# Kernel optimization log

Measured on AMD Instinct MI355X. Metric: run time of the kernel, lower is better.

The kernel has to match this reference:

```python
import jax, jax.numpy as jnp
import numpy as np

B, C, T = 8, 512, 1024
EXP = 2
E = EXP * C          # 1024, gate/value width
H, HD = 8, 64        # heads, qk head dim
QK = H * HD          # 512
AVG_LEN = 512
EPS = 1e-5


def setup_inputs() -> dict:
    key = jax.random.key(0)
    ks = jax.random.split(key, 10)
    s = 0.02
    return {
        "x": jax.random.normal(ks[0], (B, C, T), jnp.float32),
        "W_in": jax.random.normal(ks[1], (2 * E, C), jnp.float32) * s,
        "b_in": jnp.zeros((2 * E,), jnp.float32),
        "W_attn": jax.random.normal(ks[2], (QK, C), jnp.float32) * s,
        "b_attn": jnp.zeros((QK,), jnp.float32),
        "w_q": 1.0 + jax.random.normal(ks[3], (QK,), jnp.float32) * 0.1,
        "b_q": jax.random.normal(ks[4], (QK,), jnp.float32) * 0.1,
        "w_k": 1.0 + jax.random.normal(ks[5], (QK,), jnp.float32) * 0.1,
        "b_k": jax.random.normal(ks[6], (QK,), jnp.float32) * 0.1,
        "W_out": jax.random.normal(ks[7], (C, E), jnp.float32) * s,
        "b_out": jnp.zeros((C,), jnp.float32),
        "gamma": jnp.ones((C,), jnp.float32),
    }


def reference(x, W_in, b_in, W_attn, b_attn, w_q, b_q, w_k, b_k, W_out, b_out, gamma):
    residual = x
    # mlp_in (1x1 conv) + SiLU, then chunk into gate u and value v, each (B,E,T)
    uv = jax.nn.silu(jnp.einsum('oc,bct->bot', W_in, x) + b_in[:, None])
    u, v = uv[:, :E], uv[:, E:]
    # mlp_attn (1x1 conv); no activation (activation_attn unused in forward)
    z = jnp.einsum('oc,bct->bot', W_attn, x) + b_attn[:, None]  # (B,QK,T)
    # depthwise 1x1 conv on cat(z,z) = two independent per-channel affines
    q = z * w_q[:, None] + b_q[:, None]
    k = z * w_k[:, None] + b_k[:, None]
    # split heads: q,k -> (B,H,T,HD); v -> (B,H,T,E//H)
    q = q.reshape(B, H, HD, T).transpose(0, 1, 3, 2)
    k = k.reshape(B, H, HD, T).transpose(0, 1, 3, 2)
    vh = v.reshape(B, H, E // H, T).transpose(0, 1, 3, 2)
    # entropy-invariant scale: (log n / log avg_len) / sqrt(d)
    scale = (np.log(T) / np.log(AVG_LEN)) / np.sqrt(HD)
    scores = jnp.einsum('bhqd,bhkd->bhqk', q, k) * jnp.float32(scale)
    attn = jax.nn.softmax(scores, axis=-1)
    o = jnp.einsum('bhqk,bhke->bhqe', attn, vh)        # (B,H,T,E//H)
    o = o.transpose(0, 1, 3, 2).reshape(B, E, T)       # back to (B,E,T)
    # gate, project out, residual + RMSNorm over channel dim
    out = jnp.einsum('ce,bet->bct', W_out, u * o) + b_out[:, None]
    y = residual + out
    rms = jax.lax.rsqrt(jnp.mean(y * y, axis=1, keepdims=True) + EPS)
    return y * rms * gamma[:, None]
```

## Files before the change

kernel.cpp:

```cpp
#include <hip/hip_runtime.h>

typedef __attribute__((ext_vector_type(8))) short short8;
typedef __attribute__((ext_vector_type(4))) float f32x4;
typedef __attribute__((ext_vector_type(16))) float f32x16;

__device__ __forceinline__ unsigned short f2b(float f) {
  union { float f; unsigned u; } x; x.f = f;
  unsigned r = (x.u + 0x7fffu + ((x.u >> 16) & 1u)) >> 16;
  return (unsigned short)r;
}
__device__ __forceinline__ float b2f(unsigned short b) {
  union { unsigned u; float f; } x; x.u = ((unsigned)b) << 16;
  return x.f;
}
__device__ __forceinline__ unsigned cvtpk(float lo, float hi) {
  unsigned r;
  asm("v_cvt_pk_bf16_f32 %0, %1, %2" : "=v"(r) : "v"(lo), "v"(hi));
  return r;
}
__device__ __forceinline__ void plswap(unsigned& a, unsigned& b) {
  asm volatile("v_permlane32_swap_b32 %0, %1" : "+v"(a), "+v"(b));
}

#define GLDS16(gp, lp)                                                                  \
  __builtin_amdgcn_global_load_lds((const __attribute__((address_space(1))) void*)(gp), \
                                   (__attribute__((address_space(3))) void*)(lp), 16, 0, 0)

__global__ __launch_bounds__(256) void prep_kernel(const float* __restrict__ x,
                                                   const float* __restrict__ W_in,
                                                   const float* __restrict__ W_attn,
                                                   const float* __restrict__ W_out,
                                                   unsigned short* __restrict__ Wcat,
                                                   unsigned short* __restrict__ WoutB,
                                                   unsigned short* __restrict__ xT) {
  if (blockIdx.x < 4096) {
    __shared__ float tile[32][33];
    const int bid = blockIdx.x;
    const int b = bid & 7;
    const int rem = bid >> 3;
    const int c0 = (rem >> 5) << 5;
    const int t0 = (rem & 31) << 5;
    const int tj = threadIdx.x & 31, ti = threadIdx.x >> 5;
#pragma unroll
    for (int r = 0; r < 32; r += 8)
      tile[ti + r][tj] = x[(((size_t)b << 9) + c0 + ti + r) * 1024 + t0 + tj];
    __syncthreads();
#pragma unroll
    for (int r = 0; r < 32; r += 8)
      xT[(((size_t)b << 10) + t0 + ti + r) * 512 + c0 + tj] = f2b(tile[tj][ti + r]);
  } else {
    const int n1 = 2048 * 512, n2 = 512 * 512, n3 = 512 * 1024;
    for (int i = (blockIdx.x - 4096) * 256 + threadIdx.x; i < n1 + n2 + n3; i += 896 * 256) {
      if (i < n1) Wcat[i] = f2b(W_in[i]);
      else if (i < n1 + n2) Wcat[i] = f2b(W_attn[i - n1]);
      else WoutB[i - n1 - n2] = f2b(W_out[i - n1 - n2]);
    }
  }
}

__device__ __forceinline__ void gemm_stage(const unsigned short* Ag, const unsigned short* Bg,
                                           int lda, int ldb, int k0, unsigned short* lsA,
                                           unsigned short* lsB, int buf, int sr, int sk,
                                           int ldst) {
  const int bb = buf * 8192;
  GLDS16(Ag + (size_t)sr * lda + k0 + sk, (char*)lsA + bb + ldst);
  GLDS16(Ag + (size_t)(sr + 64) * lda + k0 + sk, (char*)lsA + bb + 4096 + ldst);
  GLDS16(Bg + (size_t)sr * ldb + k0 + sk, (char*)lsB + bb + ldst);
  GLDS16(Bg + (size_t)(sr + 64) * ldb + k0 + sk, (char*)lsB + bb + 4096 + ldst);
}

__device__ __forceinline__ void gemm_bt_core(const unsigned short* __restrict__ Ag,
                                             const unsigned short* __restrict__ Bg, int lda,
                                             int ldb, int K, unsigned short* lsA,
                                             unsigned short* lsB, f32x4 acc[4][4]) {
  const int tid = threadIdx.x;
  const int lane = tid & 63;
  const int w = tid >> 6;
  const int wr = w >> 1, wc = w & 1;
  const int sr = tid >> 2;
  const int sk = (((tid & 3) ^ ((sr >> 1) & 3)) << 3);
  const int ldst = (tid >> 6) << 10;

  const int nt = K >> 5;
  int c0b = 0, c1b = 1, c2b = 2;
  gemm_stage(Ag, Bg, lda, ldb, 0, lsA, lsB, 0, sr, sk, ldst);
  gemm_stage(Ag, Bg, lda, ldb, 32, lsA, lsB, 1, sr, sk, ldst);
  for (int t = 0; t < nt; ++t) {
    if (t + 1 < nt) {
      asm volatile("s_waitcnt vmcnt(4)" ::: "memory");
    } else {
      asm volatile("s_waitcnt vmcnt(0)" ::: "memory");
    }
    __builtin_amdgcn_s_barrier();
    if (t + 2 < nt)
      gemm_stage(Ag, Bg, lda, ldb, (t + 2) << 5, lsA, lsB, c2b, sr, sk, ldst);
    short8 af[4], bfr[4];
    const int bb = c0b * 8192;
    const int ko = (lane >> 4) << 4;
    const int ra = (wr << 6) + (lane & 15);
    const int rb = (wc << 6) + (lane & 15);
#pragma unroll
    for (int mi = 0; mi < 4; ++mi) {
      const int rowA = ra + (mi << 4);
      af[mi] = *(const short8*)((const char*)lsA + bb + (rowA << 6) +
                                (ko ^ (((rowA >> 1) & 3) << 4)));
    }
#pragma unroll
    for (int ni = 0; ni < 4; ++ni) {
      const int rowB = rb + (ni << 4);
      bfr[ni] = *(const short8*)((const char*)lsB + bb + (rowB << 6) +
                                 (ko ^ (((rowB >> 1) & 3) << 4)));
    }
#pragma unroll
    for (int mi = 0; mi < 4; ++mi)
#pragma unroll
      for (int ni = 0; ni < 4; ++ni)
        acc[mi][ni] =
            __builtin_amdgcn_mfma_f32_16x16x32_bf16(af[mi], bfr[ni], acc[mi][ni], 0, 0, 0);
    const int tmp = c0b; c0b = c1b; c1b = c2b; c2b = tmp;
  }
}

__global__ __launch_bounds__(256) void gemm_a_kernel(
    const unsigned short* __restrict__ Wcat, const unsigned short* __restrict__ xT,
    const float* __restrict__ b_in, const float* __restrict__ b_attn,
    const float* __restrict__ w_q, const float* __restrict__ b_q, const float* __restrict__ w_k,
    const float* __restrict__ b_k, unsigned short* __restrict__ u, unsigned short* __restrict__ v,
    unsigned short* __restrict__ qT, unsigned short* __restrict__ kT) {
  __shared__ __align__(16) unsigned short lsA[12288];
  __shared__ __align__(16) unsigned short lsB[12288];
  const int bid = ((blockIdx.x & 7) * 160) + (blockIdx.x >> 3);
  const int b = bid / 160;
  const int rem = bid % 160;
  const int m0 = (rem >> 3) << 7;
  const int n0 = (rem & 7) << 7;
  f32x4 acc[4][4];
  const f32x4 z4 = {0.f, 0.f, 0.f, 0.f};
#pragma unroll
  for (int mi = 0; mi < 4; ++mi)
#pragma unroll
    for (int ni = 0; ni < 4; ++ni) acc[mi][ni] = z4;

  const unsigned short* Ag = Wcat + (size_t)m0 * 512;
  const unsigned short* Bg = xT + ((size_t)b << 19) + ((size_t)n0 << 9);
  gemm_bt_core(Ag, Bg, 512, 512, 512, lsA, lsB, acc);

  const int lane = threadIdx.x & 63;
  const int w = threadIdx.x >> 6;
  const int wr = w >> 1, wc = w & 1;
#pragma unroll
  for (int mi = 0; mi < 4; ++mi) {
    const int row0 = m0 + (wr << 6) + (mi << 4) + ((lane >> 4) << 2);
#pragma unroll
    for (int ni = 0; ni < 4; ++ni) {
      const int col = n0 + (wc << 6) + (ni << 4) + (lane & 15);
      if (row0 < 2048) {
#pragma unroll
        for (int i = 0; i < 4; ++i) {
          const int row = row0 + i;
          const float s = acc[mi][ni][i] + b_in[row];
          const float r = s / (1.f + __expf(-s));
          if (row < 1024)
            u[((((size_t)b << 10) + row) << 10) + col] = f2b(r);
          else
            v[((((size_t)b << 10) + (row - 1024)) << 10) + col] = f2b(r);
        }
      } else {
        const int c0 = row0 - 2048;
        ushort4 qv, kv;
        unsigned short* qp = (unsigned short*)&qv;
        unsigned short* kp = (unsigned short*)&kv;
#pragma unroll
        for (int i = 0; i < 4; ++i) {
          const int c = c0 + i;
          const float z = acc[mi][ni][i] + b_attn[c];
          qp[i] = f2b(z * w_q[c] + b_q[c]);
          kp[i] = f2b(z * w_k[c] + b_k[c]);
        }
        const int h = c0 >> 6, d = c0 & 63;
        const size_t base = ((((size_t)b * 8 + h) << 10) + col) * 64 + d;
        *(ushort4*)(qT + base) = qv;
        *(ushort4*)(kT + base) = kv;
      }
    }
  }
}

__global__ __launch_bounds__(256, 2) void attn_kernel(const unsigned short* __restrict__ qT,
                                                      const unsigned short* __restrict__ kT,
                                                      const unsigned short* __restrict__ v,
                                                      const unsigned short* __restrict__ u,
                                                      unsigned short* __restrict__ uoT) {
  __shared__ __align__(16) unsigned short Kls[3 * 4096];
  __shared__ __align__(16) unsigned short Vls[3 * 8192];
  const float SCALE2 = 0.20037430567f;
  const int bx = blockIdx.x;
  const int xcd = bx & 7, idx = bx >> 3;
  const int bh = (xcd << 3) + (idx & 7);
  const int qb = idx >> 3;
  const int b = bh >> 3, h = bh & 7;
  const int tid = threadIdx.x;
  const int lane = tid & 63;
  const int w = tid >> 6;
  const int l5 = lane >> 5;
  const int l31 = lane & 31;
  const int q0 = qb << 7;

  const unsigned short* qh = qT + ((size_t)bh << 16);
  const unsigned short* kh = kT + ((size_t)bh << 16);
  const unsigned short* vh = v + ((((size_t)b << 10) + (h << 7)) << 10);

  short8 qf[4];
#pragma unroll
  for (int ds = 0; ds < 4; ++ds)
    qf[ds] = *(const short8*)(qh + (size_t)(q0 + (w << 5) + l31) * 64 + (ds << 4) + (l5 << 3));

  f32x16 o[4];
#pragma unroll
  for (int eb = 0; eb < 4; ++eb)
#pragma unroll
    for (int i = 0; i < 16; ++i) o[eb][i] = 0.f;
  float lacc = 0.f;

  const int srow = tid >> 3;
  const int scol = (((tid & 7) ^ (srow & 7)) << 3);

#define ATTN_STAGE(buf, kt)                                                            \
  {                                                                                    \
    const int t2 = (kt) << 6;                                                          \
    char* kbase = (char*)Kls + (buf)*8192;                                             \
    char* vbase = (char*)Vls + (buf)*16384;                                            \
    GLDS16(kh + (size_t)(t2 + srow) * 64 + scol, kbase + (w << 10));                   \
    GLDS16(kh + (size_t)(t2 + 32 + srow) * 64 + scol, kbase + 4096 + (w << 10));       \
    GLDS16(vh + ((size_t)srow << 10) + t2 + scol, vbase + (w << 10));                  \
    GLDS16(vh + ((size_t)(32 + srow) << 10) + t2 + scol, vbase + 4096 + (w << 10));    \
    GLDS16(vh + ((size_t)(64 + srow) << 10) + t2 + scol, vbase + 8192 + (w << 10));    \
    GLDS16(vh + ((size_t)(96 + srow) << 10) + t2 + scol, vbase + 12288 + (w << 10));   \
  }

#define KREAD(kbp, kr, ds)                                                             \
  (*(const short8*)((kbp) + ((kr) << 7) + ((((ds) << 5) + (l5 << 4)) ^ (((kr)&7) << 4))))
#define VREAD(vbp, vrow, ks)                                                           \
  (*(const short8*)((vbp) + ((vrow) << 7) + ((((ks) << 5) + (l5 << 4)) ^ (((vrow)&7) << 4))))

#define PACK(sv, out0, out1)                                                           \
  do {                                                                                 \
    float p_[16];                                                                      \
    _Pragma("unroll") for (int i_ = 0; i_ < 16; ++i_) {                                \
      p_[i_] = exp2f(sv[i_] * SCALE2);                                                 \
      lacc += p_[i_];                                                                  \
    }                                                                                  \
    unsigned W00 = cvtpk(p_[0], p_[1]), W01 = cvtpk(p_[2], p_[3]);                     \
    unsigned W10 = cvtpk(p_[4], p_[5]), W11 = cvtpk(p_[6], p_[7]);                     \
    unsigned W20 = cvtpk(p_[8], p_[9]), W21 = cvtpk(p_[10], p_[11]);                   \
    unsigned W30 = cvtpk(p_[12], p_[13]), W31 = cvtpk(p_[14], p_[15]);                 \
    unsigned a_ = W10, b_ = W00;                                                       \
    plswap(a_, b_);                                                                    \
    (out0).u4[0] = b_; (out0).u4[2] = a_;                                              \
    unsigned c_ = W11, d_ = W01;                                                       \
    plswap(c_, d_);                                                                    \
    (out0).u4[1] = d_; (out0).u4[3] = c_;                                              \
    unsigned e_ = W30, f_ = W20;                                                       \
    plswap(e_, f_);                                                                    \
    (out1).u4[0] = f_; (out1).u4[2] = e_;                                              \
    unsigned g_ = W31, h_ = W21;                                                       \
    plswap(g_, h_);                                                                    \
    (out1).u4[1] = h_; (out1).u4[3] = g_;                                              \
  } while (0)

  union U8 { short8 s8; unsigned u4[4]; };
  U8 pfP[4];

  ATTN_STAGE(0, 0);
  ATTN_STAGE(1, 1);

  asm volatile("s_waitcnt vmcnt(6)" ::: "memory");
  __builtin_amdgcn_s_barrier();
  {
    const char* kb = (const char*)Kls;
    f32x16 s0, s1;
#pragma unroll
    for (int i = 0; i < 16; ++i) { s0[i] = 0.f; s1[i] = 0.f; }
    __builtin_amdgcn_s_setprio(1);
#pragma unroll
    for (int ds = 0; ds < 4; ++ds) {
      short8 kfA = KREAD(kb, l31, ds);
      s0 = __builtin_amdgcn_mfma_f32_32x32x16_bf16(kfA, qf[ds], s0, 0, 0, 0);
      short8 kfB = KREAD(kb, 32 + l31, ds);
      s1 = __builtin_amdgcn_mfma_f32_32x32x16_bf16(kfB, qf[ds], s1, 0, 0, 0);
    }
    __builtin_amdgcn_s_setprio(0);
    PACK(s0, pfP[0], pfP[1]);
    PACK(s1, pfP[2], pfP[3]);
  }
  __builtin_amdgcn_s_barrier();
  ATTN_STAGE(2, 2);

  int ck = 1, cv = 0;
  for (int kt = 1; kt < 16; ++kt) {
    if (kt < 15) {
      asm volatile("s_waitcnt vmcnt(6)" ::: "memory");
    } else {
      asm volatile("s_waitcnt vmcnt(0)" ::: "memory");
    }
    __builtin_amdgcn_s_barrier();

    const char* kb = (const char*)Kls + ck * 8192;
    const char* vb = (const char*)Vls + cv * 16384;

    short8 kfA[4], kfB[4];
#pragma unroll
    for (int ds = 0; ds < 4; ++ds) {
      kfA[ds] = KREAD(kb, l31, ds);
      kfB[ds] = KREAD(kb, 32 + l31, ds);
    }

    f32x16 s0, s1;
#pragma unroll
    for (int i = 0; i < 16; ++i) { s0[i] = 0.f; s1[i] = 0.f; }
    __builtin_amdgcn_s_setprio(1);
#pragma unroll
    for (int ks = 0; ks < 4; ++ks) {
      s0 = __builtin_amdgcn_mfma_f32_32x32x16_bf16(kfA[ks], qf[ks], s0, 0, 0, 0);
      s1 = __builtin_amdgcn_mfma_f32_32x32x16_bf16(kfB[ks], qf[ks], s1, 0, 0, 0);
#pragma unroll
      for (int eb = 0; eb < 4; ++eb) {
        short8 vf = VREAD(vb, (eb << 5) + l31, ks);
        o[eb] = __builtin_amdgcn_mfma_f32_32x32x16_bf16(vf, pfP[ks].s8, o[eb], 0, 0, 0);
      }
    }
    __builtin_amdgcn_s_setprio(0);

    U8 pfN[4];
    PACK(s0, pfN[0], pfN[1]);
    PACK(s1, pfN[2], pfN[3]);
#pragma unroll
    for (int i = 0; i < 4; ++i) pfP[i] = pfN[i];

    if (kt + 2 < 16) {
      __builtin_amdgcn_s_barrier();
      ATTN_STAGE(cv, kt + 2);
    }
    const int third = 3 - ck - cv;
    cv = ck;
    ck = third;
  }

  {
    const char* vb = (const char*)Vls + cv * 16384;
    __builtin_amdgcn_s_setprio(1);
#pragma unroll
    for (int ks = 0; ks < 4; ++ks) {
#pragma unroll
      for (int eb = 0; eb < 4; ++eb) {
        short8 vf = VREAD(vb, (eb << 5) + l31, ks);
        o[eb] = __builtin_amdgcn_mfma_f32_32x32x16_bf16(vf, pfP[ks].s8, o[eb], 0, 0, 0);
      }
    }
    __builtin_amdgcn_s_setprio(0);
  }
#undef ATTN_STAGE
#undef KREAD
#undef VREAD
#undef PACK

  lacc += __shfl_xor(lacc, 32, 64);
  const float rl = 1.f / lacc;
  const int t = q0 + (w << 5) + l31;

#pragma unroll
  for (int eb = 0; eb < 4; ++eb) {
#pragma unroll
    for (int g = 0; g < 4; ++g) {
      const int e4 = (eb << 5) + (g << 3) + (l5 << 2);
      const int eg = (h << 7) + e4;
      ushort4 outv;
      unsigned short* op = (unsigned short*)&outv;
#pragma unroll
      for (int j = 0; j < 4; ++j) {
        const int i = (g << 2) + j;
        const float oo = o[eb][i] * rl;
        const float uu = b2f(u[((((size_t)b << 10) + eg + j) << 10) + t]);
        op[j] = f2b(oo * uu);
      }
      *(ushort4*)(uoT + ((((size_t)b << 10) + t) << 10) + eg) = outv;
    }
  }
}

__global__ __launch_bounds__(256) void gemm_c_kernel(const unsigned short* __restrict__ uoT,
                                                     const unsigned short* __restrict__ WoutB,
                                                     const float* __restrict__ x,
                                                     const float* __restrict__ b_out,
                                                     unsigned short* __restrict__ y) {
  __shared__ __align__(16) unsigned short lsA[12288];
  __shared__ __align__(16) unsigned short lsB[12288];
  const int bid = ((blockIdx.x & 7) * 32) + (blockIdx.x >> 3);
  const int b = bid >> 5;
  const int rem = bid & 31;
  const int m0 = (rem >> 2) << 7;
  const int n0 = (rem & 3) << 7;
  f32x4 acc[4][4];
  const f32x4 z4 = {0.f, 0.f, 0.f, 0.f};
#pragma unroll
  for (int mi = 0; mi < 4; ++mi)
#pragma unroll
    for (int ni = 0; ni < 4; ++ni) acc[mi][ni] = z4;

  const unsigned short* Ag = uoT + ((size_t)b << 20) + ((size_t)m0 << 10);
  const unsigned short* Bg = WoutB + ((size_t)n0 << 10);
  gemm_bt_core(Ag, Bg, 1024, 1024, 1024, lsA, lsB, acc);

  const int lane = threadIdx.x & 63;
  const int w = threadIdx.x >> 6;
  const int wr = w >> 1, wc = w & 1;
#pragma unroll
  for (int mi = 0; mi < 4; ++mi) {
    const int t4 = m0 + (wr << 6) + (mi << 4) + ((lane >> 4) << 2);
#pragma unroll
    for (int ni = 0; ni < 4; ++ni) {
      const int c = n0 + (wc << 6) + (ni << 4) + (lane & 15);
      const size_t base = ((((size_t)b << 9) + c) << 10) + t4;
      const f32x4 xv = *(const f32x4*)(x + base);
      const float bo = b_out[c];
      ushort4 ov;
      unsigned short* op = (unsigned short*)&ov;
#pragma unroll
      for (int i = 0; i < 4; ++i) op[i] = f2b(acc[mi][ni][i] + bo + xv[i]);
      *(ushort4*)(y + base) = ov;
    }
  }
}

__global__ __launch_bounds__(256) void rms_kernel(const unsigned short* __restrict__ y,
                                                  const float* __restrict__ gamma,
                                                  float* __restrict__ out) {
  __shared__ float part[8][32];
  __shared__ float rmsv[32];
  const int bid = blockIdx.x;
  const int b = bid >> 5;
  const int t0 = (bid & 31) << 5;
  const int tid = threadIdx.x;
  const int tt = tid & 31, cg = tid >> 5;
  const int t = t0 + tt;
  float vals[64];
  float ss = 0.f;
#pragma unroll
  for (int ci = 0; ci < 64; ++ci) {
    const int c = (cg << 6) + ci;
    const float vv = b2f(y[((((size_t)b << 9) + c) << 10) + t]);
    vals[ci] = vv;
    ss += vv * vv;
  }
  part[cg][tt] = ss;
  __syncthreads();
  if (tid < 32) {
    float tot = 0.f;
#pragma unroll
    for (int g = 0; g < 8; ++g) tot += part[g][tid];
    rmsv[tid] = rsqrtf(tot / 512.f + 1e-5f);
  }
  __syncthreads();
  const float rm = rmsv[tt];
#pragma unroll
  for (int ci = 0; ci < 64; ++ci) {
    const int c = (cg << 6) + ci;
    out[((((size_t)b << 9) + c) << 10) + t] = vals[ci] * rm * gamma[c];
  }
}

extern "C" void kernel_launch(void* const* d_in, const int* in_sizes, int n_in, void* d_out,
                              int out_size, void* d_ws, size_t ws_size, hipStream_t stream) {
  const float* x = (const float*)d_in[0];
  const float* W_in = (const float*)d_in[1];
  const float* b_in = (const float*)d_in[2];
  const float* W_attn = (const float*)d_in[3];
  const float* b_attn = (const float*)d_in[4];
  const float* w_q = (const float*)d_in[5];
  const float* b_q = (const float*)d_in[6];
  const float* w_k = (const float*)d_in[7];
  const float* b_k = (const float*)d_in[8];
  const float* W_out = (const float*)d_in[9];
  const float* b_out = (const float*)d_in[10];
  const float* gamma = (const float*)d_in[11];
  float* out = (float*)d_out;

  char* ws = (char*)d_ws;
  size_t off = 0;
  auto alloc = [&](size_t bytes) {
    char* p = ws + off;
    off += (bytes + 255) & ~(size_t)255;
    return p;
  };
  unsigned short* Wcat = (unsigned short*)alloc((size_t)2560 * 512 * 2);
  unsigned short* WoutB = (unsigned short*)alloc((size_t)512 * 1024 * 2);
  unsigned short* xT = (unsigned short*)alloc((size_t)8 * 1024 * 512 * 2);
  unsigned short* u = (unsigned short*)alloc((size_t)8 * 1024 * 1024 * 2);
  unsigned short* v = (unsigned short*)alloc((size_t)8 * 1024 * 1024 * 2);
  unsigned short* qT = (unsigned short*)alloc((size_t)8 * 8 * 1024 * 64 * 2);
  unsigned short* kT = (unsigned short*)alloc((size_t)8 * 8 * 1024 * 64 * 2);
  unsigned short* uoT = (unsigned short*)alloc((size_t)8 * 1024 * 1024 * 2);
  unsigned short* y = (unsigned short*)alloc((size_t)8 * 512 * 1024 * 2);
  if (off > ws_size) return;

  prep_kernel<<<4992, 256, 0, stream>>>(x, W_in, W_attn, W_out, Wcat, WoutB, xT);
  gemm_a_kernel<<<1280, 256, 0, stream>>>(Wcat, xT, b_in, b_attn, w_q, b_q, w_k, b_k, u, v, qT,
                                          kT);
  attn_kernel<<<512, 256, 0, stream>>>(qT, kT, v, u, uoT);
  gemm_c_kernel<<<256, 256, 0, stream>>>(uoT, WoutB, x, b_out, y);
  rms_kernel<<<256, 256, 0, stream>>>(y, gamma, out);
}
```

Baseline: 121.0 us.

## Rewrite input projection GEMM with 256x256 tiles, 8 waves, double-buffered K=64 stages

The fused input/attention projection GEMM is rewritten to use 256x256 output tiles with 512 threads (8 waves, each computing 128x64), K-steps of 64 with a two-buffer LDS pipeline and an XOR swizzle. It launches 320 blocks instead of 1280 128x128 blocks and raises MFMA priority with s_setprio around the math. The larger tiles are meant to raise arithmetic intensity and cut global/LDS traffic per FLOP. In exchange it uses 128KB of LDS for one block per CU and more accumulator registers, and 320 blocks may leave the 256 CUs unevenly loaded.

```diff
diff --git a/kernel.cpp b/kernel.cpp
--- a/kernel.cpp
+++ b/kernel.cpp
@@ -58,6 +58,122 @@
   }
 }
 
+__global__ __launch_bounds__(512, 1) void gemm_a_kernel(
+    const unsigned short* __restrict__ Wcat, const unsigned short* __restrict__ xT,
+    const float* __restrict__ b_in, const float* __restrict__ b_attn,
+    const float* __restrict__ w_q, const float* __restrict__ b_q, const float* __restrict__ w_k,
+    const float* __restrict__ b_k, unsigned short* __restrict__ u, unsigned short* __restrict__ v,
+    unsigned short* __restrict__ qT, unsigned short* __restrict__ kT) {
+  __shared__ __align__(16) unsigned short lsA[2][256 * 64];
+  __shared__ __align__(16) unsigned short lsB[2][256 * 64];
+  const int bid = ((blockIdx.x & 7) * 40) + (blockIdx.x >> 3);
+  const int m_tile = bid % 10;
+  const int n_tile = bid / 10;
+  const int m0 = m_tile << 8;
+  const int n0 = n_tile << 8;
+  const int tid = threadIdx.x;
+  const int lane = tid & 63;
+  const int w = tid >> 6;
+  const int wr = w >> 2, wc = w & 3;
+  const int sr = tid >> 3;
+  const int sc = (((tid & 7) ^ (sr & 7)) << 3);
+
+  const unsigned short* Ag = Wcat + (size_t)m0 * 512;
+  const unsigned short* Bg = xT + (size_t)n0 * 512;
+
+  f32x4 acc[8][4];
+#pragma unroll
+  for (int mi = 0; mi < 8; ++mi)
+#pragma unroll
+    for (int ni = 0; ni < 4; ++ni) {
+      acc[mi][ni][0] = 0.f; acc[mi][ni][1] = 0.f;
+      acc[mi][ni][2] = 0.f; acc[mi][ni][3] = 0.f;
+    }
+
+#define GA_STAGE(buf, kt)                                                              \
+  {                                                                                    \
+    const int kb = (kt) << 6;                                                          \
+    _Pragma("unroll") for (int j = 0; j < 4; ++j)                                      \
+        GLDS16(Ag + (size_t)((j << 6) + sr) * 512 + kb + sc,                           \
+               (char*)lsA[buf] + (j << 13) + (tid << 4));                              \
+    _Pragma("unroll") for (int j = 0; j < 4; ++j)                                      \
+        GLDS16(Bg + (size_t)((j << 6) + sr) * 512 + kb + sc,                           \
+               (char*)lsB[buf] + (j << 13) + (tid << 4));                              \
+  }
+
+  GA_STAGE(0, 0);
+  for (int t = 0; t < 8; ++t) {
+    asm volatile("s_waitcnt vmcnt(0)" ::: "memory");
+    __builtin_amdgcn_s_barrier();
+    if (t + 1 < 8) GA_STAGE((t + 1) & 1, t + 1);
+    const char* la = (const char*)lsA[t & 1];
+    const char* lb = (const char*)lsB[t & 1];
+#pragma unroll
+    for (int kh = 0; kh < 2; ++kh) {
+      short8 af[8], bfr[4];
+      const int sb = ((kh << 2) + (lane >> 4)) << 4;
+#pragma unroll
+      for (int mi = 0; mi < 8; ++mi) {
+        const int rowA = (wr << 7) + (mi << 4) + (lane & 15);
+        af[mi] = *(const short8*)(la + (rowA << 7) + (sb ^ ((rowA & 7) << 4)));
+      }
+#pragma unroll
+      for (int ni = 0; ni < 4; ++ni) {
+        const int rowB = (wc << 6) + (ni << 4) + (lane & 15);
+        bfr[ni] = *(const short8*)(lb + (rowB << 7) + (sb ^ ((rowB & 7) << 4)));
+      }
+      __builtin_amdgcn_s_setprio(1);
+#pragma unroll
+      for (int mi = 0; mi < 8; ++mi)
+#pragma unroll
+        for (int ni = 0; ni < 4; ++ni)
+          acc[mi][ni] =
+              __builtin_amdgcn_mfma_f32_16x16x32_bf16(af[mi], bfr[ni], acc[mi][ni], 0, 0, 0);
+      __builtin_amdgcn_s_setprio(0);
+    }
+  }
+#undef GA_STAGE
+
+  const int b = n0 >> 10;
+  const int tb = n0 & 1023;
+#pragma unroll
+  for (int mi = 0; mi < 8; ++mi) {
+    const int row0 = m0 + (wr << 7) + (mi << 4) + ((lane >> 4) << 2);
+#pragma unroll
+    for (int ni = 0; ni < 4; ++ni) {
+      const int tcol = tb + (wc << 6) + (ni << 4) + (lane & 15);
+      if (row0 < 2048) {
+#pragma unroll
+        for (int i = 0; i < 4; ++i) {
+          const int row = row0 + i;
+          const float s = acc[mi][ni][i] + b_in[row];
+          const float r = s / (1.f + __expf(-s));
+          if (row < 1024)
+            u[((((size_t)b << 10) + row) << 10) + tcol] = f2b(r);
+          else
+            v[((((size_t)b << 10) + (row - 1024)) << 10) + tcol] = f2b(r);
+        }
+      } else {
+        const int c0 = row0 - 2048;
+        ushort4 qv, kv;
+        unsigned short* qp = (unsigned short*)&qv;
+        unsigned short* kp = (unsigned short*)&kv;
+#pragma unroll
+        for (int i = 0; i < 4; ++i) {
+          const int c = c0 + i;
+          const float z = acc[mi][ni][i] + b_attn[c];
+          qp[i] = f2b(z * w_q[c] + b_q[c]);
+          kp[i] = f2b(z * w_k[c] + b_k[c]);
+        }
+        const int h = c0 >> 6, d = c0 & 63;
+        const size_t base = ((((size_t)b * 8 + h) << 10) + tcol) * 64 + d;
+        *(ushort4*)(qT + base) = qv;
+        *(ushort4*)(kT + base) = kv;
+      }
+    }
+  }
+}
+
 __device__ __forceinline__ void gemm_stage(const unsigned short* Ag, const unsigned short* Bg,
                                            int lda, int ldb, int k0, unsigned short* lsA,
                                            unsigned short* lsB, int buf, int sr, int sk,
@@ -118,71 +234,6 @@
         acc[mi][ni] =
             __builtin_amdgcn_mfma_f32_16x16x32_bf16(af[mi], bfr[ni], acc[mi][ni], 0, 0, 0);
     const int tmp = c0b; c0b = c1b; c1b = c2b; c2b = tmp;
-  }
-}
-
-__global__ __launch_bounds__(256) void gemm_a_kernel(
-    const unsigned short* __restrict__ Wcat, const unsigned short* __restrict__ xT,
-    const float* __restrict__ b_in, const float* __restrict__ b_attn,
-    const float* __restrict__ w_q, const float* __restrict__ b_q, const float* __restrict__ w_k,
-    const float* __restrict__ b_k, unsigned short* __restrict__ u, unsigned short* __restrict__ v,
-    unsigned short* __restrict__ qT, unsigned short* __restrict__ kT) {
-  __shared__ __align__(16) unsigned short lsA[12288];
-  __shared__ __align__(16) unsigned short lsB[12288];
-  const int bid = ((blockIdx.x & 7) * 160) + (blockIdx.x >> 3);
-  const int b = bid / 160;
-  const int rem = bid % 160;
-  const int m0 = (rem >> 3) << 7;
-  const int n0 = (rem & 7) << 7;
-  f32x4 acc[4][4];
-  const f32x4 z4 = {0.f, 0.f, 0.f, 0.f};
-#pragma unroll
-  for (int mi = 0; mi < 4; ++mi)
-#pragma unroll
-    for (int ni = 0; ni < 4; ++ni) acc[mi][ni] = z4;
-
-  const unsigned short* Ag = Wcat + (size_t)m0 * 512;
-  const unsigned short* Bg = xT + ((size_t)b << 19) + ((size_t)n0 << 9);
-  gemm_bt_core(Ag, Bg, 512, 512, 512, lsA, lsB, acc);
-
-  const int lane = threadIdx.x & 63;
-  const int w = threadIdx.x >> 6;
-  const int wr = w >> 1, wc = w & 1;
-#pragma unroll
-  for (int mi = 0; mi < 4; ++mi) {
-    const int row0 = m0 + (wr << 6) + (mi << 4) + ((lane >> 4) << 2);
-#pragma unroll
-    for (int ni = 0; ni < 4; ++ni) {
-      const int col = n0 + (wc << 6) + (ni << 4) + (lane & 15);
-      if (row0 < 2048) {
-#pragma unroll
-        for (int i = 0; i < 4; ++i) {
-          const int row = row0 + i;
-          const float s = acc[mi][ni][i] + b_in[row];
-          const float r = s / (1.f + __expf(-s));
-          if (row < 1024)
-            u[((((size_t)b << 10) + row) << 10) + col] = f2b(r);
-          else
-            v[((((size_t)b << 10) + (row - 1024)) << 10) + col] = f2b(r);
-        }
-      } else {
-        const int c0 = row0 - 2048;
-        ushort4 qv, kv;
-        unsigned short* qp = (unsigned short*)&qv;
-        unsigned short* kp = (unsigned short*)&kv;
-#pragma unroll
-        for (int i = 0; i < 4; ++i) {
-          const int c = c0 + i;
-          const float z = acc[mi][ni][i] + b_attn[c];
-          qp[i] = f2b(z * w_q[c] + b_q[c]);
-          kp[i] = f2b(z * w_k[c] + b_k[c]);
-        }
-        const int h = c0 >> 6, d = c0 & 63;
-        const size_t base = ((((size_t)b * 8 + h) << 10) + col) * 64 + d;
-        *(ushort4*)(qT + base) = qv;
-        *(ushort4*)(kT + base) = kv;
-      }
-    }
   }
 }
 
@@ -504,8 +555,8 @@
   if (off > ws_size) return;
 
   prep_kernel<<<4992, 256, 0, stream>>>(x, W_in, W_attn, W_out, Wcat, WoutB, xT);
-  gemm_a_kernel<<<1280, 256, 0, stream>>>(Wcat, xT, b_in, b_attn, w_q, b_q, w_k, b_k, u, v, qT,
-                                          kT);
+  gemm_a_kernel<<<320, 512, 0, stream>>>(Wcat, xT, b_in, b_attn, w_q, b_q, w_k, b_k, u, v, qT,
+                                         kT);
   attn_kernel<<<512, 256, 0, stream>>>(qT, kT, v, u, uoT);
   gemm_c_kernel<<<256, 256, 0, stream>>>(uoT, WoutB, x, b_out, y);
   rms_kernel<<<256, 256, 0, stream>>>(y, gamma, out);
```

Result: slower. 148.0 us (+22.3%).

## Enlarge first GEMM tile to 256x128 with 8 waves and MFMA priority

Applied to the files above, without the earlier changes.

The input-projection GEMM now runs 512-thread blocks that each compute a 256x128 output tile, where it used to run 256-thread blocks on 128x128 tiles. The grid is halved and the batch index is folded into the flattened token dimension. Each B tile staged in LDS is reused by twice as many rows of W, which cuts global and LDS traffic per FLOP. s_setprio is raised around the MFMA block to favour matrix issue. The costs are more LDS per block, fewer blocks to balance across CUs, and possible occupancy limits.

```diff
diff --git a/kernel.cpp b/kernel.cpp
--- a/kernel.cpp
+++ b/kernel.cpp
@@ -58,82 +58,29 @@
   }
 }
 
-__device__ __forceinline__ void gemm_stage(const unsigned short* Ag, const unsigned short* Bg,
-                                           int lda, int ldb, int k0, unsigned short* lsA,
-                                           unsigned short* lsB, int buf, int sr, int sk,
-                                           int ldst) {
-  const int bb = buf * 8192;
-  GLDS16(Ag + (size_t)sr * lda + k0 + sk, (char*)lsA + bb + ldst);
-  GLDS16(Ag + (size_t)(sr + 64) * lda + k0 + sk, (char*)lsA + bb + 4096 + ldst);
-  GLDS16(Bg + (size_t)sr * ldb + k0 + sk, (char*)lsB + bb + ldst);
-  GLDS16(Bg + (size_t)(sr + 64) * ldb + k0 + sk, (char*)lsB + bb + 4096 + ldst);
-}
-
-__device__ __forceinline__ void gemm_bt_core(const unsigned short* __restrict__ Ag,
-                                             const unsigned short* __restrict__ Bg, int lda,
-                                             int ldb, int K, unsigned short* lsA,
-                                             unsigned short* lsB, f32x4 acc[4][4]) {
-  const int tid = threadIdx.x;
-  const int lane = tid & 63;
-  const int w = tid >> 6;
-  const int wr = w >> 1, wc = w & 1;
-  const int sr = tid >> 2;
-  const int sk = (((tid & 3) ^ ((sr >> 1) & 3)) << 3);
-  const int ldst = (tid >> 6) << 10;
-
-  const int nt = K >> 5;
-  int c0b = 0, c1b = 1, c2b = 2;
-  gemm_stage(Ag, Bg, lda, ldb, 0, lsA, lsB, 0, sr, sk, ldst);
-  gemm_stage(Ag, Bg, lda, ldb, 32, lsA, lsB, 1, sr, sk, ldst);
-  for (int t = 0; t < nt; ++t) {
-    if (t + 1 < nt) {
-      asm volatile("s_waitcnt vmcnt(4)" ::: "memory");
-    } else {
-      asm volatile("s_waitcnt vmcnt(0)" ::: "memory");
-    }
-    __builtin_amdgcn_s_barrier();
-    if (t + 2 < nt)
-      gemm_stage(Ag, Bg, lda, ldb, (t + 2) << 5, lsA, lsB, c2b, sr, sk, ldst);
-    short8 af[4], bfr[4];
-    const int bb = c0b * 8192;
-    const int ko = (lane >> 4) << 4;
-    const int ra = (wr << 6) + (lane & 15);
-    const int rb = (wc << 6) + (lane & 15);
-#pragma unroll
-    for (int mi = 0; mi < 4; ++mi) {
-      const int rowA = ra + (mi << 4);
-      af[mi] = *(const short8*)((const char*)lsA + bb + (rowA << 6) +
-                                (ko ^ (((rowA >> 1) & 3) << 4)));
-    }
-#pragma unroll
-    for (int ni = 0; ni < 4; ++ni) {
-      const int rowB = rb + (ni << 4);
-      bfr[ni] = *(const short8*)((const char*)lsB + bb + (rowB << 6) +
-                                 (ko ^ (((rowB >> 1) & 3) << 4)));
-    }
-#pragma unroll
-    for (int mi = 0; mi < 4; ++mi)
-#pragma unroll
-      for (int ni = 0; ni < 4; ++ni)
-        acc[mi][ni] =
-            __builtin_amdgcn_mfma_f32_16x16x32_bf16(af[mi], bfr[ni], acc[mi][ni], 0, 0, 0);
-    const int tmp = c0b; c0b = c1b; c1b = c2b; c2b = tmp;
-  }
-}
-
-__global__ __launch_bounds__(256) void gemm_a_kernel(
+__global__ __launch_bounds__(512) void gemm_a_kernel(
     const unsigned short* __restrict__ Wcat, const unsigned short* __restrict__ xT,
     const float* __restrict__ b_in, const float* __restrict__ b_attn,
     const float* __restrict__ w_q, const float* __restrict__ b_q, const float* __restrict__ w_k,
     const float* __restrict__ b_k, unsigned short* __restrict__ u, unsigned short* __restrict__ v,
     unsigned short* __restrict__ qT, unsigned short* __restrict__ kT) {
-  __shared__ __align__(16) unsigned short lsA[12288];
-  __shared__ __align__(16) unsigned short lsB[12288];
-  const int bid = ((blockIdx.x & 7) * 160) + (blockIdx.x >> 3);
-  const int b = bid / 160;
-  const int rem = bid % 160;
-  const int m0 = (rem >> 3) << 7;
-  const int n0 = (rem & 7) << 7;
+  __shared__ __align__(16) unsigned short lsA[3 * 8192];
+  __shared__ __align__(16) unsigned short lsB[3 * 4096];
+  const int bid = ((blockIdx.x & 7) * 80) + (blockIdx.x >> 3);
+  const int n_tile = bid / 10;
+  const int m_tile = bid % 10;
+  const int m0 = m_tile << 8;
+  const int n0f = n_tile << 7;
+  const int tid = threadIdx.x;
+  const int lane = tid & 63;
+  const int w = tid >> 6;
+  const int wr = w >> 1, wc = w & 1;
+  const int sra = tid >> 2;
+  const int ska = (((tid & 3) ^ ((sra >> 1) & 3)) << 3);
+
+  const unsigned short* Ag = Wcat + (size_t)m0 * 512;
+  const unsigned short* Bg = xT + (size_t)n0f * 512;
+
   f32x4 acc[4][4];
   const f32x4 z4 = {0.f, 0.f, 0.f, 0.f};
 #pragma unroll
@@ -141,19 +88,61 @@
 #pragma unroll
     for (int ni = 0; ni < 4; ++ni) acc[mi][ni] = z4;
 
-  const unsigned short* Ag = Wcat + (size_t)m0 * 512;
-  const unsigned short* Bg = xT + ((size_t)b << 19) + ((size_t)n0 << 9);
-  gemm_bt_core(Ag, Bg, 512, 512, 512, lsA, lsB, acc);
-
-  const int lane = threadIdx.x & 63;
-  const int w = threadIdx.x >> 6;
-  const int wr = w >> 1, wc = w & 1;
+#define GA_STAGE(buf, k0)                                                              \
+  {                                                                                    \
+    GLDS16(Ag + (size_t)sra * 512 + (k0) + ska, (char*)lsA + (buf)*16384 + (tid << 4)); \
+    GLDS16(Ag + (size_t)(128 + sra) * 512 + (k0) + ska,                                \
+           (char*)lsA + (buf)*16384 + 8192 + (tid << 4));                              \
+    GLDS16(Bg + (size_t)sra * 512 + (k0) + ska, (char*)lsB + (buf)*8192 + (tid << 4)); \
+  }
+
+  int c0b = 0, c1b = 1, c2b = 2;
+  GA_STAGE(0, 0);
+  GA_STAGE(1, 32);
+  for (int t = 0; t < 16; ++t) {
+    if (t + 1 < 16) {
+      asm volatile("s_waitcnt vmcnt(3)" ::: "memory");
+    } else {
+      asm volatile("s_waitcnt vmcnt(0)" ::: "memory");
+    }
+    __builtin_amdgcn_s_barrier();
+    if (t + 2 < 16) GA_STAGE(c2b, (t + 2) << 5);
+    const char* la = (const char*)lsA + c0b * 16384;
+    const char* lb = (const char*)lsB + c0b * 8192;
+    short8 af[4], bfr[4];
+    const int ko = (lane >> 4) << 4;
+    const int ra = (wr << 6) + (lane & 15);
+    const int rb = (wc << 6) + (lane & 15);
+#pragma unroll
+    for (int mi = 0; mi < 4; ++mi) {
+      const int rowA = ra + (mi << 4);
+      af[mi] = *(const short8*)(la + (rowA << 6) + (ko ^ (((rowA >> 1) & 3) << 4)));
+    }
+#pragma unroll
+    for (int ni = 0; ni < 4; ++ni) {
+      const int rowB = rb + (ni << 4);
+      bfr[ni] = *(const short8*)(lb + (rowB << 6) + (ko ^ (((rowB >> 1) & 3) << 4)));
+    }
+    __builtin_amdgcn_s_setprio(1);
+#pragma unroll
+    for (int mi = 0; mi < 4; ++mi)
+#pragma unroll
+      for (int ni = 0; ni < 4; ++ni)
+        acc[mi][ni] =
+            __builtin_amdgcn_mfma_f32_16x16x32_bf16(af[mi], bfr[ni], acc[mi][ni], 0, 0, 0);
+    __builtin_amdgcn_s_setprio(0);
+    const int tmp = c0b; c0b = c1b; c1b = c2b; c2b = tmp;
+  }
+#undef GA_STAGE
+
+  const int b = n0f >> 10;
+  const int tb = n0f & 1023;
 #pragma unroll
   for (int mi = 0; mi < 4; ++mi) {
     const int row0 = m0 + (wr << 6) + (mi << 4) + ((lane >> 4) << 2);
 #pragma unroll
     for (int ni = 0; ni < 4; ++ni) {
-      const int col = n0 + (wc << 6) + (ni << 4) + (lane & 15);
+      const int col = tb + (wc << 6) + (ni << 4) + (lane & 15);
       if (row0 < 2048) {
 #pragma unroll
         for (int i = 0; i < 4; ++i) {
@@ -183,6 +172,69 @@
         *(ushort4*)(kT + base) = kv;
       }
     }
+  }
+}
+
+__device__ __forceinline__ void gemm_stage(const unsigned short* Ag, const unsigned short* Bg,
+                                           int lda, int ldb, int k0, unsigned short* lsA,
+                                           unsigned short* lsB, int buf, int sr, int sk,
+                                           int ldst) {
+  const int bb = buf * 8192;
+  GLDS16(Ag + (size_t)sr * lda + k0 + sk, (char*)lsA + bb + ldst);
+  GLDS16(Ag + (size_t)(sr + 64) * lda + k0 + sk, (char*)lsA + bb + 4096 + ldst);
+  GLDS16(Bg + (size_t)sr * ldb + k0 + sk, (char*)lsB + bb + ldst);
+  GLDS16(Bg + (size_t)(sr + 64) * ldb + k0 + sk, (char*)lsB + bb + 4096 + ldst);
+}
+
+__device__ __forceinline__ void gemm_bt_core(const unsigned short* __restrict__ Ag,
+                                             const unsigned short* __restrict__ Bg, int lda,
+                                             int ldb, int K, unsigned short* lsA,
+                                             unsigned short* lsB, f32x4 acc[4][4]) {
+  const int tid = threadIdx.x;
+  const int lane = tid & 63;
+  const int w = tid >> 6;
+  const int wr = w >> 1, wc = w & 1;
+  const int sr = tid >> 2;
+  const int sk = (((tid & 3) ^ ((sr >> 1) & 3)) << 3);
+  const int ldst = (tid >> 6) << 10;
+
+  const int nt = K >> 5;
+  int c0b = 0, c1b = 1, c2b = 2;
+  gemm_stage(Ag, Bg, lda, ldb, 0, lsA, lsB, 0, sr, sk, ldst);
+  gemm_stage(Ag, Bg, lda, ldb, 32, lsA, lsB, 1, sr, sk, ldst);
+  for (int t = 0; t < nt; ++t) {
+    if (t + 1 < nt) {
+      asm volatile("s_waitcnt vmcnt(4)" ::: "memory");
+    } else {
+      asm volatile("s_waitcnt vmcnt(0)" ::: "memory");
+    }
+    __builtin_amdgcn_s_barrier();
+    if (t + 2 < nt)
+      gemm_stage(Ag, Bg, lda, ldb, (t + 2) << 5, lsA, lsB, c2b, sr, sk, ldst);
+    short8 af[4], bfr[4];
+    const int bb = c0b * 8192;
+    const int ko = (lane >> 4) << 4;
+    const int ra = (wr << 6) + (lane & 15);
+    const int rb = (wc << 6) + (lane & 15);
+#pragma unroll
+    for (int mi = 0; mi < 4; ++mi) {
+      const int rowA = ra + (mi << 4);
+      af[mi] = *(const short8*)((const char*)lsA + bb + (rowA << 6) +
+                                (ko ^ (((rowA >> 1) & 3) << 4)));
+    }
+#pragma unroll
+    for (int ni = 0; ni < 4; ++ni) {
+      const int rowB = rb + (ni << 4);
+      bfr[ni] = *(const short8*)((const char*)lsB + bb + (rowB << 6) +
+                                 (ko ^ (((rowB >> 1) & 3) << 4)));
+    }
+#pragma unroll
+    for (int mi = 0; mi < 4; ++mi)
+#pragma unroll
+      for (int ni = 0; ni < 4; ++ni)
+        acc[mi][ni] =
+            __builtin_amdgcn_mfma_f32_16x16x32_bf16(af[mi], bfr[ni], acc[mi][ni], 0, 0, 0);
+    const int tmp = c0b; c0b = c1b; c1b = c2b; c2b = tmp;
   }
 }
 
@@ -504,8 +556,8 @@
   if (off > ws_size) return;
 
   prep_kernel<<<4992, 256, 0, stream>>>(x, W_in, W_attn, W_out, Wcat, WoutB, xT);
-  gemm_a_kernel<<<1280, 256, 0, stream>>>(Wcat, xT, b_in, b_attn, w_q, b_q, w_k, b_k, u, v, qT,
-                                          kT);
+  gemm_a_kernel<<<640, 512, 0, stream>>>(Wcat, xT, b_in, b_attn, w_q, b_q, w_k, b_k, u, v, qT,
+                                         kT);
   attn_kernel<<<512, 256, 0, stream>>>(qT, kT, v, u, uoT);
   gemm_c_kernel<<<256, 256, 0, stream>>>(uoT, WoutB, x, b_out, y);
   rms_kernel<<<256, 256, 0, stream>>>(y, gamma, out);
```

Result: slower. 128.1 us (+5.9%).
